# Kernel tuning notes

Measured on AMD Instinct MI355X. Metric: run time of the kernel, lower is better.

The kernel has to match this reference:

```python
import jax, jax.numpy as jnp
import numpy as np

NUM_ROI = 148
P = 1
Q = 5
N = 131072


def setup_inputs() -> dict:
    key = jax.random.key(0)
    kX, kZ, kWr, kbr, kWf, kbf = jax.random.split(key, 6)
    X = jax.random.normal(kX, (N, P), dtype=jnp.float32)
    Z = jax.random.normal(kZ, (N, Q), dtype=jnp.float32)
    # Stacked per-ROI linear layers (torch nn.Linear default init scale)
    s_r = 1.0 / np.sqrt(Q)
    s_f = 1.0 / np.sqrt(P + Q)
    Wr = jax.random.uniform(kWr, (NUM_ROI, Q), jnp.float32, -s_r, s_r)
    br = jax.random.uniform(kbr, (NUM_ROI,), jnp.float32, -s_r, s_r)
    Wf = jax.random.uniform(kWf, (NUM_ROI, P + Q), jnp.float32, -s_f, s_f)
    bf = jax.random.uniform(kbf, (NUM_ROI,), jnp.float32, -s_f, s_f)
    return {"X": X, "Z": Z, "Wr": Wr, "br": br, "Wf": Wf, "bf": bf}


def reference(X, Z, Wr, br, Wf, bf):
    # combined_XZ: [N, p+q]
    XZ = jnp.concatenate([X, Z], axis=-1)
    # All 148 per-ROI GEMVs batched into two matmuls; output stacked as [roi, N]
    r_out = jnp.einsum("nq,rq->rn", Z, Wr) + br[:, None]   # [148, N]
    f_out = jnp.einsum("nd,rd->rn", XZ, Wf) + bf[:, None]  # [148, N]
    return (r_out, f_out)
```

## Files before the change

### kernel.cpp

```cpp
#include <hip/hip_runtime.h>

#define NUM_ROI 148
#define NQ 5
#define NN 131072
#define ROI_PER 4
#define NBLK_Y (NUM_ROI / ROI_PER)
#define NBLK_X (NN / (256 * 4))

typedef float vf4 __attribute__((ext_vector_type(4)));

__global__ __launch_bounds__(256) void coconet_kernel(
    const float* __restrict__ X, const float* __restrict__ Z,
    const float* __restrict__ Wr, const float* __restrict__ br,
    const float* __restrict__ Wf, const float* __restrict__ bf,
    float* __restrict__ out)
{
    const int tid = threadIdx.x;
    const int n0 = (blockIdx.x * 256 + tid) * 4;
    const int r0 = blockIdx.y * ROI_PER;

    const vf4 x4 = *reinterpret_cast<const vf4*>(X + n0);
    const float x[4] = {x4.x, x4.y, x4.z, x4.w};

    float z[4][NQ];
    {
        const vf4* zp = reinterpret_cast<const vf4*>(Z + (size_t)n0 * NQ);
        const vf4 a = zp[0], b = zp[1], c = zp[2], d = zp[3], e = zp[4];
        const float tmp[20] = {a.x, a.y, a.z, a.w, b.x, b.y, b.z, b.w,
                               c.x, c.y, c.z, c.w, d.x, d.y, d.z, d.w,
                               e.x, e.y, e.z, e.w};
        #pragma unroll
        for (int j = 0; j < 4; ++j)
            #pragma unroll
            for (int q = 0; q < NQ; ++q) z[j][q] = tmp[j * NQ + q];
    }

    float* outR = out + (size_t)r0 * NN + n0;
    float* outF = out + (size_t)(NUM_ROI + r0) * NN + n0;

    #pragma unroll
    for (int i = 0; i < ROI_PER; ++i) {
        const int r = r0 + i;
        float wr[NQ], wf[NQ];
        #pragma unroll
        for (int q = 0; q < NQ; ++q) wr[q] = Wr[r * NQ + q];
        const float brv = br[r];
        const float wfx = Wf[r * 6 + 0];
        #pragma unroll
        for (int q = 0; q < NQ; ++q) wf[q] = Wf[r * 6 + 1 + q];
        const float bfv = bf[r];

        float rr[4], ff[4];
        #pragma unroll
        for (int j = 0; j < 4; ++j) {
            float r_ = brv;
            float f_ = fmaf(x[j], wfx, bfv);
            #pragma unroll
            for (int q = 0; q < NQ; ++q) {
                r_ = fmaf(z[j][q], wr[q], r_);
                f_ = fmaf(z[j][q], wf[q], f_);
            }
            rr[j] = r_;
            ff[j] = f_;
        }
        vf4 rv; rv.x = rr[0]; rv.y = rr[1]; rv.z = rr[2]; rv.w = rr[3];
        vf4 fv; fv.x = ff[0]; fv.y = ff[1]; fv.z = ff[2]; fv.w = ff[3];
        __builtin_nontemporal_store(rv, reinterpret_cast<vf4*>(outR + (size_t)i * NN));
        __builtin_nontemporal_store(fv, reinterpret_cast<vf4*>(outF + (size_t)i * NN));
    }
}

extern "C" void kernel_launch(void* const* d_in, const int* in_sizes, int n_in,
                              void* d_out, int out_size, void* d_ws, size_t ws_size,
                              hipStream_t stream) {
    const float* X  = (const float*)d_in[0];
    const float* Z  = (const float*)d_in[1];
    const float* Wr = (const float*)d_in[2];
    const float* br = (const float*)d_in[3];
    const float* Wf = (const float*)d_in[4];
    const float* bf = (const float*)d_in[5];
    float* out = (float*)d_out;

    dim3 grid(NBLK_X, NBLK_Y);
    coconet_kernel<<<grid, 256, 0, stream>>>(X, Z, Wr, br, Wf, bf, out);
}
```

Measured before the change: 169.0 us.

## Assign each block one output row quarter and loop over N

The grid changes from (N tiles × ROI groups) to one block per (output row, quarter of N), giving 1184 blocks that each loop 32 times over a contiguous output stretch. Each block loads only one weight set and writes one contiguous row region, which is meant to make stores more sequential and cut weight reloads. In exchange, X and Z are re-read for every output row (296 times) instead of being shared across 8 outputs per thread. That raises input traffic, which should mostly hit L2/MALL given Z is 2.6MB.

```diff
diff --git a/kernel.cpp b/kernel.cpp
--- a/kernel.cpp
+++ b/kernel.cpp
@@ -1,11 +1,10 @@
 #include <hip/hip_runtime.h>
 
 #define NUM_ROI 148
-#define NQ 5
 #define NN 131072
-#define ROI_PER 4
-#define NBLK_Y (NUM_ROI / ROI_PER)
-#define NBLK_X (NN / (256 * 4))
+#define CHUNKS_PER_ROW 4
+#define CHUNK (NN / CHUNKS_PER_ROW)
+#define NITER (CHUNK / (256 * 4))
 
 typedef float vf4 __attribute__((ext_vector_type(4)));
 
@@ -15,58 +14,40 @@
     const float* __restrict__ Wf, const float* __restrict__ bf,
     float* __restrict__ out)
 {
-    const int tid = threadIdx.x;
-    const int n0 = (blockIdx.x * 256 + tid) * 4;
-    const int r0 = blockIdx.y * ROI_PER;
+    const int id = blockIdx.x;
+    const int row = id >> 2;
+    const int quarter = id & 3;
+    const bool isF = row >= NUM_ROI;
+    const int roi = isF ? (row - NUM_ROI) : row;
 
-    const vf4 x4 = *reinterpret_cast<const vf4*>(X + n0);
-    const float x[4] = {x4.x, x4.y, x4.z, x4.w};
-
-    float z[4][NQ];
-    {
-        const vf4* zp = reinterpret_cast<const vf4*>(Z + (size_t)n0 * NQ);
-        const vf4 a = zp[0], b = zp[1], c = zp[2], d = zp[3], e = zp[4];
-        const float tmp[20] = {a.x, a.y, a.z, a.w, b.x, b.y, b.z, b.w,
-                               c.x, c.y, c.z, c.w, d.x, d.y, d.z, d.w,
-                               e.x, e.y, e.z, e.w};
-        #pragma unroll
-        for (int j = 0; j < 4; ++j)
-            #pragma unroll
-            for (int q = 0; q < NQ; ++q) z[j][q] = tmp[j * NQ + q];
+    float w0, w1, w2, w3, w4, wx, bias;
+    if (isF) {
+        wx = Wf[roi * 6 + 0];
+        w0 = Wf[roi * 6 + 1]; w1 = Wf[roi * 6 + 2]; w2 = Wf[roi * 6 + 3];
+        w3 = Wf[roi * 6 + 4]; w4 = Wf[roi * 6 + 5];
+        bias = bf[roi];
+    } else {
+        wx = 0.0f;
+        w0 = Wr[roi * 5 + 0]; w1 = Wr[roi * 5 + 1]; w2 = Wr[roi * 5 + 2];
+        w3 = Wr[roi * 5 + 3]; w4 = Wr[roi * 5 + 4];
+        bias = br[roi];
     }
 
-    float* outR = out + (size_t)r0 * NN + n0;
-    float* outF = out + (size_t)(NUM_ROI + r0) * NN + n0;
+    const int nb = quarter * CHUNK + threadIdx.x * 4;
+    float* op = out + (size_t)row * NN + nb;
 
-    #pragma unroll
-    for (int i = 0; i < ROI_PER; ++i) {
-        const int r = r0 + i;
-        float wr[NQ], wf[NQ];
-        #pragma unroll
-        for (int q = 0; q < NQ; ++q) wr[q] = Wr[r * NQ + q];
-        const float brv = br[r];
-        const float wfx = Wf[r * 6 + 0];
-        #pragma unroll
-        for (int q = 0; q < NQ; ++q) wf[q] = Wf[r * 6 + 1 + q];
-        const float bfv = bf[r];
-
-        float rr[4], ff[4];
-        #pragma unroll
-        for (int j = 0; j < 4; ++j) {
-            float r_ = brv;
-            float f_ = fmaf(x[j], wfx, bfv);
-            #pragma unroll
-            for (int q = 0; q < NQ; ++q) {
-                r_ = fmaf(z[j][q], wr[q], r_);
-                f_ = fmaf(z[j][q], wf[q], f_);
-            }
-            rr[j] = r_;
-            ff[j] = f_;
-        }
-        vf4 rv; rv.x = rr[0]; rv.y = rr[1]; rv.z = rr[2]; rv.w = rr[3];
-        vf4 fv; fv.x = ff[0]; fv.y = ff[1]; fv.z = ff[2]; fv.w = ff[3];
-        __builtin_nontemporal_store(rv, reinterpret_cast<vf4*>(outR + (size_t)i * NN));
-        __builtin_nontemporal_store(fv, reinterpret_cast<vf4*>(outF + (size_t)i * NN));
+    #pragma unroll 4
+    for (int it = 0; it < NITER; ++it) {
+        const int n = nb + it * 1024;
+        const vf4* z4 = reinterpret_cast<const vf4*>(Z + (size_t)n * 5);
+        const vf4 a = z4[0], b = z4[1], c = z4[2], d = z4[3], e = z4[4];
+        const vf4 xv = *reinterpret_cast<const vf4*>(X + n);
+        vf4 o;
+        o.x = fmaf(a.x,w0, fmaf(a.y,w1, fmaf(a.z,w2, fmaf(a.w,w3, fmaf(b.x,w4, fmaf(xv.x,wx,bias))))));
+        o.y = fmaf(b.y,w0, fmaf(b.z,w1, fmaf(b.w,w2, fmaf(c.x,w3, fmaf(c.y,w4, fmaf(xv.y,wx,bias))))));
+        o.z = fmaf(c.z,w0, fmaf(c.w,w1, fmaf(d.x,w2, fmaf(d.y,w3, fmaf(d.z,w4, fmaf(xv.z,wx,bias))))));
+        o.w = fmaf(d.w,w0, fmaf(e.x,w1, fmaf(e.y,w2, fmaf(e.z,w3, fmaf(e.w,w4, fmaf(xv.w,wx,bias))))));
+        __builtin_nontemporal_store(o, reinterpret_cast<vf4*>(op + (size_t)it * 1024));
     }
 }
 
@@ -81,6 +62,6 @@
     const float* bf = (const float*)d_in[5];
     float* out = (float*)d_out;
 
-    dim3 grid(NBLK_X, NBLK_Y);
-    coconet_kernel<<<grid, 256, 0, stream>>>(X, Z, Wr, br, Wf, bf, out);
+    const int nblocks = 2 * NUM_ROI * CHUNKS_PER_ROW;
+    coconet_kernel<<<nblocks, 256, 0, stream>>>(X, Z, Wr, br, Wf, bf, out);
 }
```

New measurement: 222.7 us. +31.8%, slower.
